# Optimization experiments

Hardware: AMD Instinct MI355X
Metric: run time of the kernel (lower is better)

Reference implementation:

```python
import jax, jax.numpy as jnp
import numpy as np

B, N, D, S = 128, 1024, 512, 64
ITERS = 3
EPS = 1e-8


def setup_inputs() -> dict:
    key = jax.random.key(0)
    ks = jax.random.split(key, 10)
    inp = {
        "inputs_pe": jax.random.normal(ks[0], (B, N, D), dtype=jnp.float32),
        "inputs": jax.random.normal(ks[1], (B, N, D), dtype=jnp.float32),
        "slots": jax.random.normal(ks[2], (1, S, D), dtype=jnp.float32),
        "W1": jax.random.normal(ks[3], (D, D), dtype=jnp.float32) * 0.02,
        "b1": jnp.zeros((D,), dtype=jnp.float32),
        "W2": jax.random.normal(ks[4], (D, D), dtype=jnp.float32) * 0.02,
        "b2": jnp.zeros((D,), dtype=jnp.float32),
        "W3": jax.random.normal(ks[5], (D, D), dtype=jnp.float32) * 0.02,
        "b3": jnp.zeros((D,), dtype=jnp.float32),
    }
    return inp


def reference(inputs_pe, inputs, slots, W1, b1, W2, b2, W3, b3):
    b = inputs_pe.shape[0]
    scale = D ** (-0.5)
    # to_k: Linear -> ReLU -> Linear -> ReLU -> Linear (torch Linear: x @ W.T + b)
    h = jax.nn.relu(jnp.einsum('bnd,ed->bne', inputs_pe, W1) + b1)
    h = jax.nn.relu(jnp.einsum('bnd,ed->bne', h, W2) + b2)
    k = jnp.einsum('bnd,ed->bne', h, W3) + b3  # [b, n, d]

    q = jnp.broadcast_to(slots, (b, S, D))  # slots never updated in the loop
    for _ in range(ITERS):
        dots = jnp.einsum('bid,bjd->bij', q, k) * scale  # [b, S, n]
        s_j = dots.sum(axis=2, keepdims=True)            # sum over keys j -> [b, S, 1]
        s_all = dots.sum(axis=(1, 2), keepdims=True)     # total per batch -> [b, 1, 1]
        dots = dots / s_j * s_all
        attn = jax.nn.sigmoid(dots)
        attn2 = attn / (attn.sum(axis=-1, keepdims=True) + EPS)
        updates = jnp.einsum('bjd,bij->bid', inputs, attn2)  # [b, S, d]
    return updates, attn
```

## Files before the change

kernel.cpp:

```cpp
#include <hip/hip_runtime.h>
#include <stdint.h>

#define Bb 128
#define Nn 1024
#define Dd 512
#define Ss 64

constexpr float kScale = 0.044194173824159216f;
constexpr float kEps = 1e-8f;

typedef __bf16 bf16x8 __attribute__((ext_vector_type(8)));
typedef float f32x4 __attribute__((ext_vector_type(4)));
typedef float f32x16 __attribute__((ext_vector_type(16)));

#define MFMA32 __builtin_amdgcn_mfma_f32_32x32x16_bf16

__device__ inline unsigned short f2bf_rne(float x) {
  unsigned u = __builtin_bit_cast(unsigned, x);
  u += 0x7FFFu + ((u >> 16) & 1u);
  return (unsigned short)(u >> 16);
}
__device__ inline float bf2f(unsigned short h) {
  unsigned u = ((unsigned)h) << 16;
  return __builtin_bit_cast(float, u);
}

__device__ inline void gl_lds16(const void* g, void* l) {
  typedef unsigned int u32;
  auto gp = (u32 __attribute__((address_space(1)))*)(unsigned long long)(uintptr_t)g;
  auto lp = (u32 __attribute__((address_space(3)))*)(unsigned int)(uintptr_t)l;
  __builtin_amdgcn_global_load_lds(gp, lp, 16, 0, 0);
}

__global__ void cast_split(const float* __restrict__ in,
                           unsigned short* __restrict__ hi,
                           unsigned short* __restrict__ lo,
                           int n4) {
  int i = blockIdx.x * blockDim.x + threadIdx.x;
  const int stride = gridDim.x * blockDim.x;
  for (; i < n4; i += stride) {
    const float4 v = ((const float4*)in)[i];
    ushort4 h, lw;
    h.x = f2bf_rne(v.x); lw.x = f2bf_rne(v.x - bf2f(h.x));
    h.y = f2bf_rne(v.y); lw.y = f2bf_rne(v.y - bf2f(h.y));
    h.z = f2bf_rne(v.z); lw.z = f2bf_rne(v.z - bf2f(h.z));
    h.w = f2bf_rne(v.w); lw.w = f2bf_rne(v.w - bf2f(h.w));
    ((ushort4*)hi)[i] = h;
    ((ushort4*)lo)[i] = lw;
  }
}

template <int ACT>
__global__ __launch_bounds__(512, 1) void gemm_8ph(
    const unsigned short* __restrict__ Ah, const unsigned short* __restrict__ Al,
    const unsigned short* __restrict__ Wh, const unsigned short* __restrict__ Wl,
    const float* __restrict__ bias,
    unsigned short* __restrict__ Ch, unsigned short* __restrict__ Cl) {
  constexpr int NT = 16;
  extern __shared__ unsigned short lds[];
  const int t = threadIdx.x, l = t & 63, w = t >> 6;
  const int wr = w >> 2, wc = w & 3;

  const int wg = ((blockIdx.x & 7) << 7) + (blockIdx.x >> 3);
  const long rowA0 = (long)(wg >> 1) * 256;
  const int colB0 = (wg & 1) * 256;

  const unsigned short* abase[4] = {Ah + rowA0 * 512, Al + rowA0 * 512,
                                    Wh + (long)colB0 * 512, Wl + (long)colB0 * 512};
  const int gsw = (l & 3) ^ ((l >> 3) & 3);
  const unsigned short* srcp[8];
  int dstp[8];
#pragma unroll
  for (int j = 0; j < 8; j++) {
    const int c = w * 8 + j;
    srcp[j] = abase[c >> 4] + ((c & 15) * 16 + (l >> 2)) * 512 + gsw * 8;
    dstp[j] = c * 512;
  }
#define STG(kt)                                                        \
  {                                                                    \
    unsigned short* bq_ = lds + ((kt) & 1) * 32768;                    \
    _Pragma("unroll") for (int j = 0; j < 8; j++)                      \
        gl_lds16(srcp[j] + (kt) * 32, bq_ + dstp[j]);                  \
  }

  const int p0 = ((l >> 5) ^ ((l >> 1) & 3)) * 8;
  int aoff[4], boff[2];
#pragma unroll
  for (int m = 0; m < 4; m++) aoff[m] = (wr * 128 + m * 32 + (l & 31)) * 32 + p0;
#pragma unroll
  for (int n = 0; n < 2; n++) boff[n] = (wc * 64 + n * 32 + (l & 31)) * 32 + p0;

  f32x16 acc[4][2] = {};
  bf16x8 ah[4], al[4], bh, bl;

#define PHASE_MFMA(NH)                                                 \
  {                                                                    \
    __builtin_amdgcn_s_barrier();                                      \
    asm volatile("s_waitcnt lgkmcnt(0)" ::: "memory");                 \
    __builtin_amdgcn_sched_barrier(0);                                 \
    __builtin_amdgcn_s_setprio(1);                                     \
    _Pragma("unroll") for (int m = 0; m < 4; m++) {                    \
      acc[m][NH] = MFMA32(ah[m], bh, acc[m][NH], 0, 0, 0);             \
      acc[m][NH] = MFMA32(al[m], bh, acc[m][NH], 0, 0, 0);             \
      acc[m][NH] = MFMA32(ah[m], bl, acc[m][NH], 0, 0, 0);             \
    }                                                                  \
    __builtin_amdgcn_s_setprio(0);                                     \
  }

  STG(0);

  for (int kt = 0; kt < NT; ++kt) {
    const unsigned short* bq = lds + (kt & 1) * 32768;
    asm volatile("s_waitcnt vmcnt(0)" ::: "memory");
    __builtin_amdgcn_s_barrier();
    __builtin_amdgcn_sched_barrier(0);
#pragma unroll
    for (int m = 0; m < 4; m++) {
      ah[m] = *(const bf16x8*)(bq + aoff[m]);
      al[m] = *(const bf16x8*)(bq + 8192 + aoff[m]);
    }
    bh = *(const bf16x8*)(bq + 16384 + boff[0]);
    bl = *(const bf16x8*)(bq + 24576 + boff[0]);
    if (kt + 1 < NT) STG(kt + 1);
    PHASE_MFMA(0)
    __builtin_amdgcn_s_barrier();
    __builtin_amdgcn_sched_barrier(0);
    bh = *(const bf16x8*)(bq + 16384 + boff[1]);
    bl = *(const bf16x8*)(bq + 24576 + boff[1]);
    PHASE_MFMA(1)
    __builtin_amdgcn_s_barrier();
    __builtin_amdgcn_sched_barrier(0);
#pragma unroll
    for (int m = 0; m < 4; m++) {
      ah[m] = *(const bf16x8*)(bq + (aoff[m] ^ 16));
      al[m] = *(const bf16x8*)(bq + 8192 + (aoff[m] ^ 16));
    }
    bh = *(const bf16x8*)(bq + 16384 + (boff[0] ^ 16));
    bl = *(const bf16x8*)(bq + 24576 + (boff[0] ^ 16));
    PHASE_MFMA(0)
    __builtin_amdgcn_s_barrier();
    __builtin_amdgcn_sched_barrier(0);
    bh = *(const bf16x8*)(bq + 16384 + (boff[1] ^ 16));
    bl = *(const bf16x8*)(bq + 24576 + (boff[1] ^ 16));
    PHASE_MFMA(1)
  }
#undef STG
#undef PHASE_MFMA

#pragma unroll
  for (int m = 0; m < 4; m++)
#pragma unroll
    for (int n = 0; n < 2; n++) {
      const int col = colB0 + wc * 64 + n * 32 + (l & 31);
      const float bv = bias[col];
#pragma unroll
      for (int r = 0; r < 16; r++) {
        const long row = rowA0 + wr * 128 + m * 32 + (r & 3) + 8 * (r >> 2) + 4 * (l >> 5);
        float xv = acc[m][n][r] + bv;
        if (ACT) xv = fmaxf(xv, 0.0f);
        const unsigned short h = f2bf_rne(xv);
        const long idx = row * 512 + col;
        Ch[idx] = h;
        Cl[idx] = f2bf_rne(xv - bf2f(h));
      }
    }
}

__global__ __launch_bounds__(256) void gemm_dots_split(
    const unsigned short* __restrict__ Qh, const unsigned short* __restrict__ Ql,
    const unsigned short* __restrict__ Kh, const unsigned short* __restrict__ Kl,
    float* __restrict__ dots) {
  constexpr int K = 512, BM = 64, BN = 128, BK = 32;
  __shared__ __align__(16) unsigned short lah[BM * BK];
  __shared__ __align__(16) unsigned short lal[BM * BK];
  __shared__ __align__(16) unsigned short lbh[BN * BK];
  __shared__ __align__(16) unsigned short lbl[BN * BK];
  const int t = threadIdx.x, l = t & 63, w = t >> 6;
  const int b = blockIdx.x >> 3, bc = blockIdx.x & 7;
  const unsigned short* kh = Kh + (long)b * Nn * Dd;
  const unsigned short* kl = Kl + (long)b * Nn * Dd;
  f32x4 acc[4][2] = {};

  for (int k0 = 0; k0 < K; k0 += BK) {
    {
      const int c = t;
      const int ga = (c >> 2) * K + k0 + (c & 3) * 8;
      const int lo = (w * 64) * 8;
      gl_lds16(Qh + ga, lah + lo);
      gl_lds16(Ql + ga, lal + lo);
    }
#pragma unroll
    for (int qq = 0; qq < 2; qq++) {
      const int c = qq * 256 + t;
      const long gb = (long)(bc * BN + (c >> 2)) * K + k0 + (c & 3) * 8;
      const int lo = (qq * 256 + w * 64) * 8;
      gl_lds16(kh + gb, lbh + lo);
      gl_lds16(kl + gb, lbl + lo);
    }
    __syncthreads();
    bf16x8 ah[4], al[4], bh[2], bl[2];
#pragma unroll
    for (int m = 0; m < 4; m++) {
      const int off = (m * 16 + (l & 15)) * BK + (l >> 4) * 8;
      ah[m] = *(const bf16x8*)(lah + off);
      al[m] = *(const bf16x8*)(lal + off);
    }
#pragma unroll
    for (int n = 0; n < 2; n++) {
      const int off = (w * 32 + n * 16 + (l & 15)) * BK + (l >> 4) * 8;
      bh[n] = *(const bf16x8*)(lbh + off);
      bl[n] = *(const bf16x8*)(lbl + off);
    }
#pragma unroll
    for (int m = 0; m < 4; m++)
#pragma unroll
      for (int n = 0; n < 2; n++) {
        acc[m][n] = __builtin_amdgcn_mfma_f32_16x16x32_bf16(ah[m], bh[n], acc[m][n], 0, 0, 0);
        acc[m][n] = __builtin_amdgcn_mfma_f32_16x16x32_bf16(al[m], bh[n], acc[m][n], 0, 0, 0);
        acc[m][n] = __builtin_amdgcn_mfma_f32_16x16x32_bf16(ah[m], bl[n], acc[m][n], 0, 0, 0);
      }
    __syncthreads();
  }
  float* dp = dots + (long)b * Ss * Nn;
#pragma unroll
  for (int m = 0; m < 4; m++) {
    const int row = m * 16 + (l >> 4) * 4;
#pragma unroll
    for (int n = 0; n < 2; n++) {
      const int col = bc * BN + w * 32 + n * 16 + (l & 15);
#pragma unroll
      for (int r = 0; r < 4; r++) dp[(long)(row + r) * Nn + col] = acc[m][n][r] * kScale;
    }
  }
}

__global__ __launch_bounds__(256) void reduce_k(
    const float* __restrict__ dots, float* __restrict__ s_j, float* __restrict__ s_all) {
  const int b = blockIdx.x;
  const int t = threadIdx.x;
  const float* dp = dots + (long)b * Ss * Nn;
  const int i = t >> 2, qq = t & 3;
  float s = 0.f;
  const float* rp = dp + i * Nn + qq * 256;
  for (int j = 0; j < 256; j++) s += rp[j];
  __shared__ float part[256];
  __shared__ float rowsum[64];
  part[t] = s;
  __syncthreads();
  if (t < 64) {
    const float v = part[t * 4] + part[t * 4 + 1] + part[t * 4 + 2] + part[t * 4 + 3];
    rowsum[t] = v;
    s_j[b * 64 + t] = v;
  }
  __syncthreads();
  if (t == 0) {
    float tot = 0.f;
    for (int k = 0; k < 64; k++) tot += rowsum[k];
    s_all[b] = tot;
  }
}

__global__ __launch_bounds__(256) void attn_k(
    const float* __restrict__ dots, const float* __restrict__ s_j,
    const float* __restrict__ s_all, float* __restrict__ attn_out,
    float* __restrict__ inv_r) {
  const int bi = blockIdx.x;
  const int b = bi >> 6;
  const int t = threadIdx.x;
  const float ratio = s_all[b] / s_j[bi];
  const float* dp = dots + (long)bi * Nn;
  float* ap = attn_out + (long)bi * Nn;
  float s = 0.f;
#pragma unroll
  for (int qq = 0; qq < 4; qq++) {
    const int j = qq * 256 + t;
    const float x = dp[j] * ratio;
    const float a = 1.f / (1.f + expf(-x));
    ap[j] = a;
    s += a;
  }
  __shared__ float red[256];
  red[t] = s;
  __syncthreads();
  for (int off = 128; off > 0; off >>= 1) {
    if (t < off) red[t] += red[t + off];
    __syncthreads();
  }
  if (t == 0) inv_r[bi] = 1.f / (red[0] + kEps);
}

__global__ __launch_bounds__(256, 1) void updates_k2(
    const float* __restrict__ attn, const float* __restrict__ inputs,
    const float* __restrict__ inv_r, float* __restrict__ out0) {
  constexpr int NT2 = 32;
  constexpr int BUF_F = 10240;
  extern __shared__ float ldsf[];
  const int t = threadIdx.x, lam = t & 63, w = t >> 6;
  const int b = blockIdx.x >> 1, dt = blockIdx.x & 1;
  const int ig = t >> 5, dg = t & 31;
  const float* inb = inputs + (size_t)b * (Nn * Dd) + dt * 256;
  const float* attsrc = attn + (size_t)b * (Ss * Nn) + (size_t)(t >> 2) * Nn + (t & 3) * 8;
  float acc[8][8] = {};
  float4 ga0, ga1, gb0, gb1;

#define UISSUE(bufi, tile, G0, G1)                                        \
  {                                                                       \
    const int j0_ = (tile)*32;                                            \
    G0 = *(const float4*)(attsrc + j0_);                                  \
    G1 = *(const float4*)(attsrc + j0_ + 4);                              \
    float* db_ = ldsf + (bufi)*BUF_F;                                     \
    _Pragma("unroll") for (int i_ = 0; i_ < 8; i_++) {                    \
      const int row_ = i_ * 4 + w;                                        \
      gl_lds16(inb + (size_t)(j0_ + row_) * Dd + lam * 4, db_ + row_ * 256); \
    }                                                                     \
  }

#define UWRITE(bufi, G0, G1)                                              \
  {                                                                       \
    float* ab_ = ldsf + (bufi)*BUF_F + 8192;                              \
    const int col_ = t >> 2;                                              \
    const int r0_ = (t & 3) * 8;                                          \
    ab_[(r0_ + 0) * 64 + col_] = G0.x;                                    \
    ab_[(r0_ + 1) * 64 + col_] = G0.y;                                    \
    ab_[(r0_ + 2) * 64 + col_] = G0.z;                                    \
    ab_[(r0_ + 3) * 64 + col_] = G0.w;                                    \
    ab_[(r0_ + 4) * 64 + col_] = G1.x;                                    \
    ab_[(r0_ + 5) * 64 + col_] = G1.y;                                    \
    ab_[(r0_ + 6) * 64 + col_] = G1.z;                                    \
    ab_[(r0_ + 7) * 64 + col_] = G1.w;                                    \
  }

#define UCOMP(bufi)                                                       \
  {                                                                       \
    const float* db_ = ldsf + (bufi)*BUF_F;                               \
    const float* ab_ = db_ + 8192;                                        \
    _Pragma("unroll 4") for (int jj = 0; jj < 32; jj++) {                 \
      float av[8], vv[8];                                                 \
      *(float4*)&av[0] = *(const float4*)(ab_ + jj * 64 + ig * 8);        \
      *(float4*)&av[4] = *(const float4*)(ab_ + jj * 64 + ig * 8 + 4);    \
      *(float4*)&vv[0] = *(const float4*)(db_ + jj * 256 + dg * 8);       \
      *(float4*)&vv[4] = *(const float4*)(db_ + jj * 256 + dg * 8 + 4);   \
      _Pragma("unroll") for (int m_ = 0; m_ < 8; m_++)                    \
          _Pragma("unroll") for (int n_ = 0; n_ < 8; n_++)                \
              acc[m_][n_] = __builtin_fmaf(av[m_], vv[n_], acc[m_][n_]);  \
    }                                                                     \
  }

  UISSUE(0, 0, ga0, ga1);
  UISSUE(1, 1, gb0, gb1);
  UWRITE(0, ga0, ga1);

  for (int tt = 0; tt < NT2; tt += 2) {
    asm volatile("s_waitcnt vmcnt(10)" ::: "memory");
    UWRITE((tt + 1) % 3, gb0, gb1);
    asm volatile("s_waitcnt lgkmcnt(0)" ::: "memory");
    __builtin_amdgcn_s_barrier();
    __builtin_amdgcn_sched_barrier(0);
    if (tt < NT2 - 2) UISSUE((tt + 2) % 3, tt + 2, ga0, ga1);
    UCOMP(tt % 3);
    if (tt + 1 < NT2 - 1) {
      asm volatile("s_waitcnt vmcnt(10)" ::: "memory");
    } else {
      asm volatile("s_waitcnt vmcnt(0)" ::: "memory");
    }
    if (tt + 1 < NT2 - 1) UWRITE((tt + 2) % 3, ga0, ga1);
    asm volatile("s_waitcnt lgkmcnt(0)" ::: "memory");
    __builtin_amdgcn_s_barrier();
    __builtin_amdgcn_sched_barrier(0);
    if (tt + 1 < NT2 - 2) UISSUE((tt + 3) % 3, tt + 3, gb0, gb1);
    UCOMP((tt + 1) % 3);
  }
#undef UISSUE
#undef UWRITE
#undef UCOMP

#pragma unroll
  for (int m = 0; m < 8; m++) {
    const int i = ig * 8 + m;
    const float ir = inv_r[b * 64 + i];
    float4 o0, o1;
    o0.x = acc[m][0] * ir; o0.y = acc[m][1] * ir; o0.z = acc[m][2] * ir; o0.w = acc[m][3] * ir;
    o1.x = acc[m][4] * ir; o1.y = acc[m][5] * ir; o1.z = acc[m][6] * ir; o1.w = acc[m][7] * ir;
    float* op = out0 + (size_t)(b * 64 + i) * Dd + dt * 256 + dg * 8;
    *(float4*)op = o0;
    *(float4*)(op + 4) = o1;
  }
}

extern "C" void kernel_launch(void* const* d_in, const int* in_sizes, int n_in,
                              void* d_out, int out_size, void* d_ws, size_t ws_size,
                              hipStream_t stream) {
  (void)in_sizes; (void)n_in; (void)out_size; (void)ws_size;
  const float* inputs_pe = (const float*)d_in[0];
  const float* inputs = (const float*)d_in[1];
  const float* slots = (const float*)d_in[2];
  const float* W1 = (const float*)d_in[3];
  const float* b1 = (const float*)d_in[4];
  const float* W2 = (const float*)d_in[5];
  const float* b2 = (const float*)d_in[6];
  const float* W3 = (const float*)d_in[7];
  const float* b3 = (const float*)d_in[8];

  char* ws = (char*)d_ws;
  size_t off = 0;
  auto alloc = [&](size_t bytes) -> void* {
    void* p = ws + off;
    off += (bytes + 255) & ~(size_t)255;
    return p;
  };
  const size_t actB = (size_t)Bb * Nn * Dd * 2;
  unsigned short* Ahi = (unsigned short*)alloc(actB);
  unsigned short* Alo = (unsigned short*)alloc(actB);
  unsigned short* Bhi = (unsigned short*)alloc(actB);
  unsigned short* Blo = (unsigned short*)alloc(actB);
  unsigned short* w1h = (unsigned short*)alloc(Dd * Dd * 2);
  unsigned short* w1l = (unsigned short*)alloc(Dd * Dd * 2);
  unsigned short* w2h = (unsigned short*)alloc(Dd * Dd * 2);
  unsigned short* w2l = (unsigned short*)alloc(Dd * Dd * 2);
  unsigned short* w3h = (unsigned short*)alloc(Dd * Dd * 2);
  unsigned short* w3l = (unsigned short*)alloc(Dd * Dd * 2);
  unsigned short* sh = (unsigned short*)alloc(Ss * Dd * 2);
  unsigned short* sl = (unsigned short*)alloc(Ss * Dd * 2);
  float* dotsb = (float*)alloc((size_t)Bb * Ss * Nn * 4);
  float* s_j = (float*)alloc(Bb * Ss * 4);
  float* s_all = (float*)alloc(Bb * 4);
  float* inv_r = (float*)alloc(Bb * Ss * 4);

  float* out_updates = (float*)d_out;
  float* out_attn = out_updates + (size_t)Bb * Ss * Dd;

  const int kLdsG = 2 * 64 * 1024;
  const int kLdsU = 3 * 40 * 1024;
  hipFuncSetAttribute(reinterpret_cast<const void*>(gemm_8ph<1>),
                      hipFuncAttributeMaxDynamicSharedMemorySize, kLdsG);
  hipFuncSetAttribute(reinterpret_cast<const void*>(gemm_8ph<0>),
                      hipFuncAttributeMaxDynamicSharedMemorySize, kLdsG);
  hipFuncSetAttribute(reinterpret_cast<const void*>(updates_k2),
                      hipFuncAttributeMaxDynamicSharedMemorySize, kLdsU);

  cast_split<<<4096, 256, 0, stream>>>(inputs_pe, Ahi, Alo, Bb * Nn * Dd / 4);
  cast_split<<<256, 256, 0, stream>>>(W1, w1h, w1l, Dd * Dd / 4);
  cast_split<<<256, 256, 0, stream>>>(W2, w2h, w2l, Dd * Dd / 4);
  cast_split<<<256, 256, 0, stream>>>(W3, w3h, w3l, Dd * Dd / 4);
  cast_split<<<32, 256, 0, stream>>>(slots, sh, sl, Ss * Dd / 4);

  gemm_8ph<1><<<1024, 512, kLdsG, stream>>>(Ahi, Alo, w1h, w1l, b1, Bhi, Blo);
  gemm_8ph<1><<<1024, 512, kLdsG, stream>>>(Bhi, Blo, w2h, w2l, b2, Ahi, Alo);
  gemm_8ph<0><<<1024, 512, kLdsG, stream>>>(Ahi, Alo, w3h, w3l, b3, Bhi, Blo);

  gemm_dots_split<<<Bb * 8, 256, 0, stream>>>(sh, sl, Bhi, Blo, dotsb);
  reduce_k<<<Bb, 256, 0, stream>>>(dotsb, s_j, s_all);
  attn_k<<<Bb * Ss, 256, 0, stream>>>(dotsb, s_j, s_all, out_attn, inv_r);
  updates_k2<<<Bb * 2, 256, kLdsU, stream>>>(out_attn, inputs, inv_r, out_updates);
}
```

Measured before the change: 1.074 ms.

## Restructure split-bf16 GEMM into 4-stage half-K pipeline with register double-buffering

Replaces the 2-stage, 32-wide K tile GEMM with a 4-deep ring of 16-wide K stages loaded three stages ahead, using partial vmcnt waits instead of draining all loads each iteration. LDS fragments are double-buffered in registers so the next stage's reads overlap the current MFMA cluster, and there is one barrier per stage instead of four per K tile. This is meant to hide global-load latency and cut synchronisation stalls in the three MLP GEMMs. The cost is more VGPR pressure from the duplicated fragment sets and more finely tuned waitcnt logic that could be fragile.

```diff
diff --git a/kernel.cpp b/kernel.cpp
--- a/kernel.cpp
+++ b/kernel.cpp
@@ -51,12 +51,12 @@
 }
 
 template <int ACT>
-__global__ __launch_bounds__(512, 1) void gemm_8ph(
+__global__ __launch_bounds__(512, 1) void gemm_hp(
     const unsigned short* __restrict__ Ah, const unsigned short* __restrict__ Al,
     const unsigned short* __restrict__ Wh, const unsigned short* __restrict__ Wl,
     const float* __restrict__ bias,
     unsigned short* __restrict__ Ch, unsigned short* __restrict__ Cl) {
-  constexpr int NT = 16;
+  constexpr int NH = 32;
   extern __shared__ unsigned short lds[];
   const int t = threadIdx.x, l = t & 63, w = t >> 6;
   const int wr = w >> 2, wc = w & 3;
@@ -65,87 +65,85 @@
   const long rowA0 = (long)(wg >> 1) * 256;
   const int colB0 = (wg & 1) * 256;
 
-  const unsigned short* abase[4] = {Ah + rowA0 * 512, Al + rowA0 * 512,
-                                    Wh + (long)colB0 * 512, Wl + (long)colB0 * 512};
-  const int gsw = (l & 3) ^ ((l >> 3) & 3);
-  const unsigned short* srcp[8];
-  int dstp[8];
-#pragma unroll
-  for (int j = 0; j < 8; j++) {
-    const int c = w * 8 + j;
-    srcp[j] = abase[c >> 4] + ((c & 15) * 16 + (l >> 2)) * 512 + gsw * 8;
-    dstp[j] = c * 512;
-  }
-#define STG(kt)                                                        \
-  {                                                                    \
-    unsigned short* bq_ = lds + ((kt) & 1) * 32768;                    \
-    _Pragma("unroll") for (int j = 0; j < 8; j++)                      \
-        gl_lds16(srcp[j] + (kt) * 32, bq_ + dstp[j]);                  \
-  }
-
-  const int p0 = ((l >> 5) ^ ((l >> 1) & 3)) * 8;
-  int aoff[4], boff[2];
-#pragma unroll
-  for (int m = 0; m < 4; m++) aoff[m] = (wr * 128 + m * 32 + (l & 31)) * 32 + p0;
-#pragma unroll
-  for (int n = 0; n < 2; n++) boff[n] = (wc * 64 + n * 32 + (l & 31)) * 32 + p0;
+  const unsigned short* sbase =
+      (w < 4) ? ((w < 2) ? Ah + rowA0 * 512 : Al + rowA0 * 512)
+              : ((w < 6) ? Wh + (long)colB0 * 512 : Wl + (long)colB0 * 512);
+  const int lcb = (w & 1) * 4;
+  const int gsw = (l & 1) ^ ((l >> 3) & 1);
+  const unsigned short* src0 = sbase + (lcb * 32 + (l >> 1)) * 512 + gsw * 8;
+  const int dst0 = (w >> 1) * 4096 + lcb * 512;
+
+#define STG(h)                                                            \
+  {                                                                       \
+    unsigned short* bq_ = lds + ((h) & 3) * 16384;                        \
+    _Pragma("unroll") for (int j = 0; j < 4; j++)                         \
+        gl_lds16(src0 + j * 16384 + (h) * 16, bq_ + dst0 + j * 512);      \
+  }
+
+  const int p8 = ((l >> 5) ^ ((l >> 2) & 1)) * 8;
+  const int abase0 = (wr * 128 + (l & 31)) * 16 + p8;
+  const int bbase0 = 8192 + (wc * 64 + (l & 31)) * 16 + p8;
+
+#define READF(h, S)                                                       \
+  {                                                                       \
+    const unsigned short* bq_ = lds + ((h) & 3) * 16384;                  \
+    _Pragma("unroll") for (int m = 0; m < 4; m++) {                       \
+      ah##S[m] = *(const bf16x8*)(bq_ + abase0 + m * 512);                \
+      al##S[m] = *(const bf16x8*)(bq_ + 4096 + abase0 + m * 512);         \
+    }                                                                     \
+    _Pragma("unroll") for (int n = 0; n < 2; n++) {                       \
+      bh##S[n] = *(const bf16x8*)(bq_ + bbase0 + n * 512);                \
+      bl##S[n] = *(const bf16x8*)(bq_ + 4096 + bbase0 + n * 512);         \
+    }                                                                     \
+  }
+
+#define MFMACL(S)                                                         \
+  {                                                                       \
+    _Pragma("unroll") for (int m = 0; m < 4; m++)                         \
+        _Pragma("unroll") for (int n = 0; n < 2; n++) {                   \
+      acc[m][n] = MFMA32(ah##S[m], bh##S[n], acc[m][n], 0, 0, 0);         \
+      acc[m][n] = MFMA32(al##S[m], bh##S[n], acc[m][n], 0, 0, 0);         \
+      acc[m][n] = MFMA32(ah##S[m], bl##S[n], acc[m][n], 0, 0, 0);         \
+    }                                                                     \
+  }
+
+#define BODY(h, CUR, NXT)                                                 \
+  {                                                                       \
+    asm volatile("s_waitcnt lgkmcnt(0)" ::: "memory");                    \
+    __builtin_amdgcn_sched_barrier(0);                                    \
+    if ((h) < 29) {                                                       \
+      asm volatile("s_waitcnt vmcnt(8)" ::: "memory");                    \
+    } else if ((h) == 29) {                                               \
+      asm volatile("s_waitcnt vmcnt(4)" ::: "memory");                    \
+    } else if ((h) == 30) {                                               \
+      asm volatile("s_waitcnt vmcnt(0)" ::: "memory");                    \
+    }                                                                     \
+    __builtin_amdgcn_s_barrier();                                         \
+    if ((h) + 4 < NH) STG((h) + 4);                                       \
+    if ((h) + 1 < NH) READF((h) + 1, NXT);                                \
+    __builtin_amdgcn_sched_barrier(0);                                    \
+    __builtin_amdgcn_s_setprio(1);                                        \
+    MFMACL(CUR);                                                          \
+    __builtin_amdgcn_s_setprio(0);                                        \
+  }
 
   f32x16 acc[4][2] = {};
-  bf16x8 ah[4], al[4], bh, bl;
-
-#define PHASE_MFMA(NH)                                                 \
-  {                                                                    \
-    __builtin_amdgcn_s_barrier();                                      \
-    asm volatile("s_waitcnt lgkmcnt(0)" ::: "memory");                 \
-    __builtin_amdgcn_sched_barrier(0);                                 \
-    __builtin_amdgcn_s_setprio(1);                                     \
-    _Pragma("unroll") for (int m = 0; m < 4; m++) {                    \
-      acc[m][NH] = MFMA32(ah[m], bh, acc[m][NH], 0, 0, 0);             \
-      acc[m][NH] = MFMA32(al[m], bh, acc[m][NH], 0, 0, 0);             \
-      acc[m][NH] = MFMA32(ah[m], bl, acc[m][NH], 0, 0, 0);             \
-    }                                                                  \
-    __builtin_amdgcn_s_setprio(0);                                     \
-  }
-
-  STG(0);
-
-  for (int kt = 0; kt < NT; ++kt) {
-    const unsigned short* bq = lds + (kt & 1) * 32768;
-    asm volatile("s_waitcnt vmcnt(0)" ::: "memory");
-    __builtin_amdgcn_s_barrier();
-    __builtin_amdgcn_sched_barrier(0);
-#pragma unroll
-    for (int m = 0; m < 4; m++) {
-      ah[m] = *(const bf16x8*)(bq + aoff[m]);
-      al[m] = *(const bf16x8*)(bq + 8192 + aoff[m]);
-    }
-    bh = *(const bf16x8*)(bq + 16384 + boff[0]);
-    bl = *(const bf16x8*)(bq + 24576 + boff[0]);
-    if (kt + 1 < NT) STG(kt + 1);
-    PHASE_MFMA(0)
-    __builtin_amdgcn_s_barrier();
-    __builtin_amdgcn_sched_barrier(0);
-    bh = *(const bf16x8*)(bq + 16384 + boff[1]);
-    bl = *(const bf16x8*)(bq + 24576 + boff[1]);
-    PHASE_MFMA(1)
-    __builtin_amdgcn_s_barrier();
-    __builtin_amdgcn_sched_barrier(0);
-#pragma unroll
-    for (int m = 0; m < 4; m++) {
-      ah[m] = *(const bf16x8*)(bq + (aoff[m] ^ 16));
-      al[m] = *(const bf16x8*)(bq + 8192 + (aoff[m] ^ 16));
-    }
-    bh = *(const bf16x8*)(bq + 16384 + (boff[0] ^ 16));
-    bl = *(const bf16x8*)(bq + 24576 + (boff[0] ^ 16));
-    PHASE_MFMA(0)
-    __builtin_amdgcn_s_barrier();
-    __builtin_amdgcn_sched_barrier(0);
-    bh = *(const bf16x8*)(bq + 16384 + (boff[1] ^ 16));
-    bl = *(const bf16x8*)(bq + 24576 + (boff[1] ^ 16));
-    PHASE_MFMA(1)
+  bf16x8 ahA[4], alA[4], bhA[2], blA[2];
+  bf16x8 ahB[4], alB[4], bhB[2], blB[2];
+
+  STG(0); STG(1); STG(2); STG(3);
+  asm volatile("s_waitcnt vmcnt(12)" ::: "memory");
+  __builtin_amdgcn_s_barrier();
+  READF(0, A);
+
+  for (int hh = 0; hh < NH; hh += 2) {
+    BODY(hh, A, B);
+    BODY(hh + 1, B, A);
   }
 #undef STG
-#undef PHASE_MFMA
+#undef READF
+#undef MFMACL
+#undef BODY
 
 #pragma unroll
   for (int m = 0; m < 4; m++)
@@ -429,11 +427,11 @@
   float* out_updates = (float*)d_out;
   float* out_attn = out_updates + (size_t)Bb * Ss * Dd;
 
-  const int kLdsG = 2 * 64 * 1024;
+  const int kLdsG = 4 * 32 * 1024;
   const int kLdsU = 3 * 40 * 1024;
-  hipFuncSetAttribute(reinterpret_cast<const void*>(gemm_8ph<1>),
+  hipFuncSetAttribute(reinterpret_cast<const void*>(gemm_hp<1>),
                       hipFuncAttributeMaxDynamicSharedMemorySize, kLdsG);
-  hipFuncSetAttribute(reinterpret_cast<const void*>(gemm_8ph<0>),
+  hipFuncSetAttribute(reinterpret_cast<const void*>(gemm_hp<0>),
                       hipFuncAttributeMaxDynamicSharedMemorySize, kLdsG);
   hipFuncSetAttribute(reinterpret_cast<const void*>(updates_k2),
                       hipFuncAttributeMaxDynamicSharedMemorySize, kLdsU);
@@ -444,9 +442,9 @@
   cast_split<<<256, 256, 0, stream>>>(W3, w3h, w3l, Dd * Dd / 4);
   cast_split<<<32, 256, 0, stream>>>(slots, sh, sl, Ss * Dd / 4);
 
-  gemm_8ph<1><<<1024, 512, kLdsG, stream>>>(Ahi, Alo, w1h, w1l, b1, Bhi, Blo);
-  gemm_8ph<1><<<1024, 512, kLdsG, stream>>>(Bhi, Blo, w2h, w2l, b2, Ahi, Alo);
-  gemm_8ph<0><<<1024, 512, kLdsG, stream>>>(Ahi, Alo, w3h, w3l, b3, Bhi, Blo);
+  gemm_hp<1><<<1024, 512, kLdsG, stream>>>(Ahi, Alo, w1h, w1l, b1, Bhi, Blo);
+  gemm_hp<1><<<1024, 512, kLdsG, stream>>>(Bhi, Blo, w2h, w2l, b2, Ahi, Alo);
+  gemm_hp<0><<<1024, 512, kLdsG, stream>>>(Ahi, Alo, w3h, w3l, b3, Bhi, Blo);
 
   gemm_dots_split<<<Bb * 8, 256, 0, stream>>>(sh, sl, Bhi, Blo, dotsb);
   reduce_k<<<Bb, 256, 0, stream>>>(dotsb, s_j, s_all);
```

Result: slower. 1.107 ms (+3.1%).
